# Kernel optimization log

Measured on AMD Instinct MI355X. Metric: run time of the kernel, lower is better.

## Reference

```python
import jax, jax.numpy as jnp
import numpy as np

DEPTH = 12
NODE_SIZE = 64
IN_SCALE = 1.0
SCALE = 0.1
IN_W = 1.8
SIZE = 2 ** DEPTH - 1          # 4095 total nodes
REST = SIZE - 1                # 4094 non-root nodes
M_BATCH = 128


def setup_inputs() -> dict:
    key = jax.random.key(0)
    k1, k2, k3 = jax.random.split(key, 3)
    weights = IN_W + 1e-4 * jax.random.normal(k1, (SIZE,), dtype=jnp.float32)
    noise_root = jax.random.normal(k2, (M_BATCH, NODE_SIZE, 1), dtype=jnp.float32)
    noise_rest = jax.random.normal(k3, (M_BATCH, NODE_SIZE, REST), dtype=jnp.float32)
    return {"weights": weights, "noise_root": noise_root, "noise_rest": noise_rest, "M": M_BATCH}


def reference(weights, noise_root, noise_rest, M):
    # Root: Normal(0, in_scale).rsample((M, node_size, 1))
    root = IN_SCALE * noise_root                      # (M, node, 1)
    samples_levels = [root]
    m_levels = []
    scale_levels = []
    off = 0
    for d in range(1, DEPTH):
        n = 2 ** d
        w = jax.nn.sigmoid(weights[off:off + n])       # (n,)
        parent = jnp.arange(n) // 2                    # half-index parent lookup
        m = w[None, None, :] * samples_levels[-1][:, :, parent]   # (M, node, n)
        sc = jnp.broadcast_to(((1.0 - w) * SCALE)[None, None, :], m.shape)
        samp = m + sc * noise_rest[:, :, off:off + n]  # reparameterized rsample
        samples_levels.append(samp)
        m_levels.append(m)
        scale_levels.append(sc)
        off += n
    samples = jnp.concatenate(samples_levels[::-1], axis=2)  # (M, node, 4095)
    ms = jnp.concatenate(m_levels[::-1], axis=2)              # (M, node, 4094)
    scales = jnp.concatenate(scale_levels[::-1], axis=2)      # (M, node, 4094)
    return samples, ms, scales
```

## Files before the change

### kernel.cpp

```cpp
#include <hip/hip_runtime.h>


constexpr int   kRows  = 8192;
constexpr float kScale = 0.1f;

typedef float f4_ __attribute__((ext_vector_type(4)));
typedef float f2_ __attribute__((ext_vector_type(2)));
typedef f4_ f4u __attribute__((aligned(4)));
typedef f2_ f2u __attribute__((aligned(4)));

__device__ __align__(16) float2 g_tab[4096];

__global__ __launch_bounds__(256) void lgt_precompute(
    const float* __restrict__ weights)
{
    int t = blockIdx.x * 256 + threadIdx.x;
    if (t < 4094) {
        int d = 31 - __clz(t + 2);
        int c = t + 4098 - 3 * (1 << d);
        float w = 1.0f / (1.0f + __expf(-weights[t]));
        g_tab[c] = make_float2(w, (1.0f - w) * kScale);
    }
}

__device__ __forceinline__ void lgkm_barrier() {
    __builtin_amdgcn_sched_barrier(0);
    asm volatile("s_waitcnt lgkmcnt(0)" ::: "memory");
    __builtin_amdgcn_s_barrier();
    __builtin_amdgcn_sched_barrier(0);
}

__global__ __launch_bounds__(256) void lgt_main(
    const float* __restrict__ noise_root,
    const float* __restrict__ noise_rest,
    float* __restrict__ samples,
    float* __restrict__ ms,
    float* __restrict__ scales)
{
    __shared__ float sL[256];

    const int row = blockIdx.x;
    const int tid = threadIdx.x;
    const float* __restrict__ nr = noise_rest + (size_t)row * 4094;
    float* __restrict__ sr = samples + (size_t)row * 4095;
    float* __restrict__ mr = ms      + (size_t)row * 4094;
    float* __restrict__ cr = scales  + (size_t)row * 4094;

    const float nzs = nr[tid];
    const float n8  = nr[254 + tid];
    const f2_  n9   = *(const f2_*)(nr + 510 + 2 * tid);
    const f2_  nA0  = *(const f2_*)(nr + 1022 + 4 * tid);
    const f2_  nA1  = *(const f2_*)(nr + 1022 + 4 * tid + 2);
    f2_ nL[4];
    #pragma unroll
    for (int k = 0; k < 4; ++k)
        nL[k] = *(const f2_*)(nr + 2046 + 8 * tid + 2 * k);
    const float rootv = noise_root[row];

    if (tid == 0) { sL[254] = rootv; sr[4094] = rootv; }
    lgkm_barrier();

    #pragma unroll
    for (int d = 1; d <= 7; ++d) {
        const int off     = (1 << d) - 2;
        const int n       = 1 << d;
        const int colbase = 4096 - (n << 1);
        if (tid >= off && tid < off + n) {
            const int c = colbase + (tid - off);
            const float2 t2 = g_tab[c];
            const float  p  = sL[(c >> 1) - 1792];
            const float  mv = t2.x * p;
            const float  v  = fmaf(t2.y, nzs, mv);
            sL[c - 3840] = v;
            sr[c] = v; mr[c] = mv; cr[c] = t2.y;
        }
        lgkm_barrier();
    }

    const float a7 = sL[tid >> 1];

    const float2 t8 = g_tab[3584 + tid];
    const float  m8 = t8.x * a7;
    const float  v8 = fmaf(t8.y, n8, m8);
    sr[3584 + tid] = v8; mr[3584 + tid] = m8; cr[3584 + tid] = t8.y;

    const f4_ t9 = *(const f4_*)(&g_tab[3072 + 2 * tid]);
    const float m90 = t9.x * v8, m91 = t9.z * v8;
    const float v90 = fmaf(t9.y, n9.x, m90);
    const float v91 = fmaf(t9.w, n9.y, m91);
    {
        f2_ sv; sv.x = v90; sv.y = v91;
        f2_ mv; mv.x = m90; mv.y = m91;
        f2_ cv; cv.x = t9.y; cv.y = t9.w;
        *(f2u*)(sr + 3072 + 2 * tid) = sv;
        *(f2_*)(mr + 3072 + 2 * tid) = mv;
        *(f2_*)(cr + 3072 + 2 * tid) = cv;
    }

    const f4_ tA = *(const f4_*)(&g_tab[2048 + 4 * tid]);
    const f4_ tB = *(const f4_*)(&g_tab[2048 + 4 * tid + 2]);
    const float mA0 = tA.x * v90, mA1 = tA.z * v90;
    const float mB0 = tB.x * v91, mB1 = tB.z * v91;
    const float vA0 = fmaf(tA.y, nA0.x, mA0);
    const float vA1 = fmaf(tA.w, nA0.y, mA1);
    const float vB0 = fmaf(tB.y, nA1.x, mB0);
    const float vB1 = fmaf(tB.w, nA1.y, mB1);
    {
        f4_ sv; sv.x = vA0; sv.y = vA1; sv.z = vB0; sv.w = vB1;
        f4_ mv; mv.x = mA0; mv.y = mA1; mv.z = mB0; mv.w = mB1;
        f4_ cv; cv.x = tA.y; cv.y = tA.w; cv.z = tB.y; cv.w = tB.w;
        *(f4u*)(sr + 2048 + 4 * tid) = sv;
        *(f4u*)(mr + 2048 + 4 * tid) = mv;
        *(f4u*)(cr + 2048 + 4 * tid) = cv;
    }

    const float pv0 = vA0, pv1 = vA1, pv2 = vB0, pv3 = vB1;
    float sv[8], mv[8], cv[8];
    #pragma unroll
    for (int k = 0; k < 4; ++k) {
        const f4_  t = *(const f4_*)(&g_tab[8 * tid + 2 * k]);
        const float p = (k == 0) ? pv0 : (k == 1) ? pv1 : (k == 2) ? pv2 : pv3;
        const float m0 = t.x * p, m1 = t.z * p;
        sv[2 * k]     = fmaf(t.y, nL[k].x, m0);
        sv[2 * k + 1] = fmaf(t.w, nL[k].y, m1);
        mv[2 * k] = m0; mv[2 * k + 1] = m1;
        cv[2 * k] = t.y; cv[2 * k + 1] = t.w;
    }
    {
        f4_ a, b;
        a.x = sv[0]; a.y = sv[1]; a.z = sv[2]; a.w = sv[3];
        b.x = sv[4]; b.y = sv[5]; b.z = sv[6]; b.w = sv[7];
        *(f4u*)(sr + 8 * tid)     = a;
        *(f4u*)(sr + 8 * tid + 4) = b;
        a.x = mv[0]; a.y = mv[1]; a.z = mv[2]; a.w = mv[3];
        b.x = mv[4]; b.y = mv[5]; b.z = mv[6]; b.w = mv[7];
        *(f4u*)(mr + 8 * tid)     = a;
        *(f4u*)(mr + 8 * tid + 4) = b;
        a.x = cv[0]; a.y = cv[1]; a.z = cv[2]; a.w = cv[3];
        b.x = cv[4]; b.y = cv[5]; b.z = cv[6]; b.w = cv[7];
        *(f4u*)(cr + 8 * tid)     = a;
        *(f4u*)(cr + 8 * tid + 4) = b;
    }
}

extern "C" void kernel_launch(void* const* d_in, const int* in_sizes, int n_in,
                              void* d_out, int out_size, void* d_ws, size_t ws_size,
                              hipStream_t stream)
{
    const float* weights    = (const float*)d_in[0];
    const float* noise_root = (const float*)d_in[1];
    const float* noise_rest = (const float*)d_in[2];

    float* out     = (float*)d_out;
    float* samples = out;
    float* ms      = samples + (size_t)kRows * 4095;
    float* scales  = ms      + (size_t)kRows * 4094;

    lgt_precompute<<<(4094 + 255) / 256, 256, 0, stream>>>(weights);
    lgt_main<<<kRows, 256, 0, stream>>>(noise_root, noise_rest,
                                        samples, ms, scales);
}
```

Measured before the change: 120.3 us.

## Fuse sigmoid precompute into main kernel and process four rows per block

Removes the separate precompute kernel and its global table. Each thread now computes the sigmoid weights and scales for its own columns in registers. Each block processes four rows so that per-thread setup is shared across them, which removes one launch and the table loads. In exchange, each block runs the barrier-heavy top-level chain four times in sequence, and there are a quarter as many blocks to hide latency with.

```diff
diff --git a/kernel.cpp b/kernel.cpp
--- a/kernel.cpp
+++ b/kernel.cpp
@@ -1,26 +1,17 @@
 #include <hip/hip_runtime.h>
 
 
-constexpr int   kRows  = 8192;
-constexpr float kScale = 0.1f;
+constexpr int   kRows   = 8192;
+constexpr int   kRPB    = 4;
+constexpr float kScale  = 0.1f;
 
 typedef float f4_ __attribute__((ext_vector_type(4)));
 typedef float f2_ __attribute__((ext_vector_type(2)));
 typedef f4_ f4u __attribute__((aligned(4)));
 typedef f2_ f2u __attribute__((aligned(4)));
 
-__device__ __align__(16) float2 g_tab[4096];
-
-__global__ __launch_bounds__(256) void lgt_precompute(
-    const float* __restrict__ weights)
-{
-    int t = blockIdx.x * 256 + threadIdx.x;
-    if (t < 4094) {
-        int d = 31 - __clz(t + 2);
-        int c = t + 4098 - 3 * (1 << d);
-        float w = 1.0f / (1.0f + __expf(-weights[t]));
-        g_tab[c] = make_float2(w, (1.0f - w) * kScale);
-    }
+__device__ __forceinline__ float sigm(float x) {
+    return 1.0f / (1.0f + __expf(-x));
 }
 
 __device__ __forceinline__ void lgkm_barrier() {
@@ -30,7 +21,8 @@
     __builtin_amdgcn_sched_barrier(0);
 }
 
-__global__ __launch_bounds__(256) void lgt_main(
+__global__ __launch_bounds__(256) void lgt_fused(
+    const float* __restrict__ weights,
     const float* __restrict__ noise_root,
     const float* __restrict__ noise_rest,
     float* __restrict__ samples,
@@ -38,108 +30,132 @@
     float* __restrict__ scales)
 {
     __shared__ float sL[256];
+    const int tid = threadIdx.x;
 
-    const int row = blockIdx.x;
-    const int tid = threadIdx.x;
-    const float* __restrict__ nr = noise_rest + (size_t)row * 4094;
-    float* __restrict__ sr = samples + (size_t)row * 4095;
-    float* __restrict__ mr = ms      + (size_t)row * 4094;
-    float* __restrict__ cr = scales  + (size_t)row * 4094;
+    const float wA  = sigm(weights[tid < 254 ? tid : 0]);
+    const float scA = (1.0f - wA) * kScale;
 
-    const float nzs = nr[tid];
-    const float n8  = nr[254 + tid];
-    const f2_  n9   = *(const f2_*)(nr + 510 + 2 * tid);
-    const f2_  nA0  = *(const f2_*)(nr + 1022 + 4 * tid);
-    const f2_  nA1  = *(const f2_*)(nr + 1022 + 4 * tid + 2);
-    f2_ nL[4];
+    const float wt8  = weights[254 + tid];
+    const f2_  wt9  = *(const f2_*)(weights + 510 + 2 * tid);
+    const f2_  wtA0 = *(const f2_*)(weights + 1022 + 4 * tid);
+    const f2_  wtA1 = *(const f2_*)(weights + 1022 + 4 * tid + 2);
+    f2_ wtB[4];
     #pragma unroll
     for (int k = 0; k < 4; ++k)
-        nL[k] = *(const f2_*)(nr + 2046 + 8 * tid + 2 * k);
-    const float rootv = noise_root[row];
+        wtB[k] = *(const f2_*)(weights + 2046 + 8 * tid + 2 * k);
 
-    if (tid == 0) { sL[254] = rootv; sr[4094] = rootv; }
-    lgkm_barrier();
-
+    const float w8 = sigm(wt8),   c8 = (1.0f - w8) * kScale;
+    const float w90 = sigm(wt9.x), c90 = (1.0f - w90) * kScale;
+    const float w91 = sigm(wt9.y), c91 = (1.0f - w91) * kScale;
+    const float wa0 = sigm(wtA0.x), ca0 = (1.0f - wa0) * kScale;
+    const float wa1 = sigm(wtA0.y), ca1 = (1.0f - wa1) * kScale;
+    const float wa2 = sigm(wtA1.x), ca2 = (1.0f - wa2) * kScale;
+    const float wa3 = sigm(wtA1.y), ca3 = (1.0f - wa3) * kScale;
+    float wb[8], cb[8];
     #pragma unroll
-    for (int d = 1; d <= 7; ++d) {
-        const int off     = (1 << d) - 2;
-        const int n       = 1 << d;
-        const int colbase = 4096 - (n << 1);
-        if (tid >= off && tid < off + n) {
-            const int c = colbase + (tid - off);
-            const float2 t2 = g_tab[c];
-            const float  p  = sL[(c >> 1) - 1792];
-            const float  mv = t2.x * p;
-            const float  v  = fmaf(t2.y, nzs, mv);
-            sL[c - 3840] = v;
-            sr[c] = v; mr[c] = mv; cr[c] = t2.y;
-        }
-        lgkm_barrier();
+    for (int k = 0; k < 4; ++k) {
+        wb[2 * k]     = sigm(wtB[k].x); cb[2 * k]     = (1.0f - wb[2 * k]) * kScale;
+        wb[2 * k + 1] = sigm(wtB[k].y); cb[2 * k + 1] = (1.0f - wb[2 * k + 1]) * kScale;
     }
 
-    const float a7 = sL[tid >> 1];
+    const int row0 = blockIdx.x * kRPB;
 
-    const float2 t8 = g_tab[3584 + tid];
-    const float  m8 = t8.x * a7;
-    const float  v8 = fmaf(t8.y, n8, m8);
-    sr[3584 + tid] = v8; mr[3584 + tid] = m8; cr[3584 + tid] = t8.y;
+    for (int rr = 0; rr < kRPB; ++rr) {
+        const int row = row0 + rr;
+        const float* __restrict__ nr = noise_rest + (size_t)row * 4094;
+        float* __restrict__ sr = samples + (size_t)row * 4095;
+        float* __restrict__ mr = ms      + (size_t)row * 4094;
+        float* __restrict__ cr = scales  + (size_t)row * 4094;
 
-    const f4_ t9 = *(const f4_*)(&g_tab[3072 + 2 * tid]);
-    const float m90 = t9.x * v8, m91 = t9.z * v8;
-    const float v90 = fmaf(t9.y, n9.x, m90);
-    const float v91 = fmaf(t9.w, n9.y, m91);
-    {
-        f2_ sv; sv.x = v90; sv.y = v91;
-        f2_ mv; mv.x = m90; mv.y = m91;
-        f2_ cv; cv.x = t9.y; cv.y = t9.w;
-        *(f2u*)(sr + 3072 + 2 * tid) = sv;
-        *(f2_*)(mr + 3072 + 2 * tid) = mv;
-        *(f2_*)(cr + 3072 + 2 * tid) = cv;
-    }
+        const float nzs = nr[tid];
+        const float n8  = nr[254 + tid];
+        const f2_  n9   = *(const f2_*)(nr + 510 + 2 * tid);
+        const f2_  nA0  = *(const f2_*)(nr + 1022 + 4 * tid);
+        const f2_  nA1  = *(const f2_*)(nr + 1022 + 4 * tid + 2);
+        f2_ nL[4];
+        #pragma unroll
+        for (int k = 0; k < 4; ++k)
+            nL[k] = *(const f2_*)(nr + 2046 + 8 * tid + 2 * k);
+        const float rootv = noise_root[row];
 
-    const f4_ tA = *(const f4_*)(&g_tab[2048 + 4 * tid]);
-    const f4_ tB = *(const f4_*)(&g_tab[2048 + 4 * tid + 2]);
-    const float mA0 = tA.x * v90, mA1 = tA.z * v90;
-    const float mB0 = tB.x * v91, mB1 = tB.z * v91;
-    const float vA0 = fmaf(tA.y, nA0.x, mA0);
-    const float vA1 = fmaf(tA.w, nA0.y, mA1);
-    const float vB0 = fmaf(tB.y, nA1.x, mB0);
-    const float vB1 = fmaf(tB.w, nA1.y, mB1);
-    {
-        f4_ sv; sv.x = vA0; sv.y = vA1; sv.z = vB0; sv.w = vB1;
-        f4_ mv; mv.x = mA0; mv.y = mA1; mv.z = mB0; mv.w = mB1;
-        f4_ cv; cv.x = tA.y; cv.y = tA.w; cv.z = tB.y; cv.w = tB.w;
-        *(f4u*)(sr + 2048 + 4 * tid) = sv;
-        *(f4u*)(mr + 2048 + 4 * tid) = mv;
-        *(f4u*)(cr + 2048 + 4 * tid) = cv;
-    }
+        if (tid == 0) { sL[254] = rootv; sr[4094] = rootv; }
+        lgkm_barrier();
 
-    const float pv0 = vA0, pv1 = vA1, pv2 = vB0, pv3 = vB1;
-    float sv[8], mv[8], cv[8];
-    #pragma unroll
-    for (int k = 0; k < 4; ++k) {
-        const f4_  t = *(const f4_*)(&g_tab[8 * tid + 2 * k]);
-        const float p = (k == 0) ? pv0 : (k == 1) ? pv1 : (k == 2) ? pv2 : pv3;
-        const float m0 = t.x * p, m1 = t.z * p;
-        sv[2 * k]     = fmaf(t.y, nL[k].x, m0);
-        sv[2 * k + 1] = fmaf(t.w, nL[k].y, m1);
-        mv[2 * k] = m0; mv[2 * k + 1] = m1;
-        cv[2 * k] = t.y; cv[2 * k + 1] = t.w;
-    }
-    {
-        f4_ a, b;
-        a.x = sv[0]; a.y = sv[1]; a.z = sv[2]; a.w = sv[3];
-        b.x = sv[4]; b.y = sv[5]; b.z = sv[6]; b.w = sv[7];
-        *(f4u*)(sr + 8 * tid)     = a;
-        *(f4u*)(sr + 8 * tid + 4) = b;
-        a.x = mv[0]; a.y = mv[1]; a.z = mv[2]; a.w = mv[3];
-        b.x = mv[4]; b.y = mv[5]; b.z = mv[6]; b.w = mv[7];
-        *(f4u*)(mr + 8 * tid)     = a;
-        *(f4u*)(mr + 8 * tid + 4) = b;
-        a.x = cv[0]; a.y = cv[1]; a.z = cv[2]; a.w = cv[3];
-        b.x = cv[4]; b.y = cv[5]; b.z = cv[6]; b.w = cv[7];
-        *(f4u*)(cr + 8 * tid)     = a;
-        *(f4u*)(cr + 8 * tid + 4) = b;
+        #pragma unroll
+        for (int d = 1; d <= 7; ++d) {
+            const int off     = (1 << d) - 2;
+            const int n       = 1 << d;
+            const int colbase = 4096 - (n << 1);
+            if (tid >= off && tid < off + n) {
+                const int c = colbase + (tid - off);
+                const float p  = sL[(c >> 1) - 1792];
+                const float mv = wA * p;
+                const float v  = fmaf(scA, nzs, mv);
+                sL[c - 3840] = v;
+                sr[c] = v; mr[c] = mv; cr[c] = scA;
+            }
+            lgkm_barrier();
+        }
+
+        const float a7 = sL[tid >> 1];
+
+        const float m8 = w8 * a7;
+        const float v8 = fmaf(c8, n8, m8);
+        sr[3584 + tid] = v8; mr[3584 + tid] = m8; cr[3584 + tid] = c8;
+
+        const float m90 = w90 * v8, m91 = w91 * v8;
+        const float v90 = fmaf(c90, n9.x, m90);
+        const float v91 = fmaf(c91, n9.y, m91);
+        {
+            f2_ sv; sv.x = v90; sv.y = v91;
+            f2_ mv; mv.x = m90; mv.y = m91;
+            f2_ cv; cv.x = c90; cv.y = c91;
+            *(f2u*)(sr + 3072 + 2 * tid) = sv;
+            *(f2_*)(mr + 3072 + 2 * tid) = mv;
+            *(f2_*)(cr + 3072 + 2 * tid) = cv;
+        }
+
+        const float mA0 = wa0 * v90, mA1 = wa1 * v90;
+        const float mA2 = wa2 * v91, mA3 = wa3 * v91;
+        const float vA0 = fmaf(ca0, nA0.x, mA0);
+        const float vA1 = fmaf(ca1, nA0.y, mA1);
+        const float vA2 = fmaf(ca2, nA1.x, mA2);
+        const float vA3 = fmaf(ca3, nA1.y, mA3);
+        {
+            f4_ sv; sv.x = vA0; sv.y = vA1; sv.z = vA2; sv.w = vA3;
+            f4_ mv; mv.x = mA0; mv.y = mA1; mv.z = mA2; mv.w = mA3;
+            f4_ cv; cv.x = ca0; cv.y = ca1; cv.z = ca2; cv.w = ca3;
+            *(f4u*)(sr + 2048 + 4 * tid) = sv;
+            *(f4u*)(mr + 2048 + 4 * tid) = mv;
+            *(f4u*)(cr + 2048 + 4 * tid) = cv;
+        }
+
+        const float pv[4] = { vA0, vA1, vA2, vA3 };
+        float sv[8], mv[8], cv[8];
+        #pragma unroll
+        for (int k = 0; k < 4; ++k) {
+            const float p  = pv[k];
+            const float m0 = wb[2 * k] * p, m1 = wb[2 * k + 1] * p;
+            sv[2 * k]     = fmaf(cb[2 * k],     nL[k].x, m0);
+            sv[2 * k + 1] = fmaf(cb[2 * k + 1], nL[k].y, m1);
+            mv[2 * k] = m0;          mv[2 * k + 1] = m1;
+            cv[2 * k] = cb[2 * k];   cv[2 * k + 1] = cb[2 * k + 1];
+        }
+        {
+            f4_ a, b;
+            a.x = sv[0]; a.y = sv[1]; a.z = sv[2]; a.w = sv[3];
+            b.x = sv[4]; b.y = sv[5]; b.z = sv[6]; b.w = sv[7];
+            *(f4u*)(sr + 8 * tid)     = a;
+            *(f4u*)(sr + 8 * tid + 4) = b;
+            a.x = mv[0]; a.y = mv[1]; a.z = mv[2]; a.w = mv[3];
+            b.x = mv[4]; b.y = mv[5]; b.z = mv[6]; b.w = mv[7];
+            *(f4u*)(mr + 8 * tid)     = a;
+            *(f4u*)(mr + 8 * tid + 4) = b;
+            a.x = cv[0]; a.y = cv[1]; a.z = cv[2]; a.w = cv[3];
+            b.x = cv[4]; b.y = cv[5]; b.z = cv[6]; b.w = cv[7];
+            *(f4u*)(cr + 8 * tid)     = a;
+            *(f4u*)(cr + 8 * tid + 4) = b;
+        }
     }
 }
 
@@ -156,7 +172,6 @@
     float* ms      = samples + (size_t)kRows * 4095;
     float* scales  = ms      + (size_t)kRows * 4094;
 
-    lgt_precompute<<<(4094 + 255) / 256, 256, 0, stream>>>(weights);
-    lgt_main<<<kRows, 256, 0, stream>>>(noise_root, noise_rest,
-                                        samples, ms, scales);
+    lgt_fused<<<kRows / kRPB, 256, 0, stream>>>(weights, noise_root, noise_rest,
+                                                samples, ms, scales);
 }
```

New measurement: 123.7 us. +2.8%, slower.
